# Kernel tuning notes

Hardware: AMD Instinct MI355X
Metric: run time of the kernel (lower is better)

The kernel has to match this reference:

```python
import jax, jax.numpy as jnp
import numpy as np

N = 100000      # nodes (single node type)
R = 4           # relations
E = 800000      # edges per relation (avg in-degree ~32)
D_IN, D_H, D_OUT = 256, 64, 16


def setup_inputs() -> dict:
    key = jax.random.key(0)
    ks = jax.random.split(key, 9)
    x = jax.random.normal(ks[0], (N, D_IN), dtype=jnp.float32)
    src = jax.random.randint(ks[1], (R, E), 0, N, dtype=jnp.int32)
    dst = jax.random.randint(ks[2], (R, E), 0, N, dtype=jnp.int32)
    s_in = 1.0 / np.sqrt(D_IN)
    s_h = 1.0 / np.sqrt(D_H)
    W1 = jax.random.normal(ks[3], (R, D_IN, D_H), dtype=jnp.float32) * s_in
    L1w = jax.random.normal(ks[4], (D_IN, D_H), dtype=jnp.float32) * s_in
    L1b = jnp.zeros((D_H,), dtype=jnp.float32)
    W2 = jax.random.normal(ks[5], (R, D_H, D_OUT), dtype=jnp.float32) * s_h
    L2w = jax.random.normal(ks[6], (D_H, D_OUT), dtype=jnp.float32) * s_h
    L2b = jnp.zeros((D_OUT,), dtype=jnp.float32)
    return {"x": x, "src": src, "dst": dst, "W1": W1, "L1w": L1w,
            "L1b": L1b, "W2": W2, "L2w": L2w, "L2b": L2b}


def _rel_graph_conv(h, src, dst, W):
    """Per-relation GEMM + gather + scatter-add + right-normalize, summed over relations.
    h: [N, d_in]; src/dst: [R, E]; W: [R, d_in, d_out] -> [N, d_out]
    """
    hw = jnp.einsum('nd,rdh->rnh', h, W)  # transform first (d_out small), then gather

    def agg(hr, s, d):
        deg = jax.ops.segment_sum(jnp.ones((E,), hr.dtype), d, num_segments=N)
        msg = jax.ops.segment_sum(hr[s], d, num_segments=N)  # [N, d_out]
        return msg / jnp.maximum(deg, 1.0)[:, None]          # norm='right'

    return jnp.sum(jax.vmap(agg)(hw, src, dst), axis=0)


def reference(x, src, dst, W1, L1w, L1b, W2, L2w, L2b):
    # Layer 1: relation conv + self-loop linear + ReLU (dropout = eval/identity)
    h = _rel_graph_conv(x, src, dst, W1) + x @ L1w + L1b
    h = jax.nn.relu(h)
    # Layer 2: no activation
    out = _rel_graph_conv(h, src, dst, W2) + h @ L2w + L2b
    return out
```

## Files before the change

kernel.cpp:

```cpp
#include <hip/hip_runtime.h>


constexpr int NN = 100000, RR = 4, EE = 800000;
constexpr int RE = RR * EE;
constexpr int NBKT = (NN + 63) / 64;
constexpr int BCAP = 3072;
constexpr int NG1 = (NN + 63) / 64;
constexpr int CHUNK = 8192;
constexpr int NB = (RE + CHUNK - 1) / CHUNK;
constexpr int EPT = CHUNK / 512;

typedef short bf16x8 __attribute__((ext_vector_type(8)));
typedef float f32x4 __attribute__((ext_vector_type(4)));

__device__ inline unsigned short f2bf(float f) {
  unsigned u = __float_as_uint(f);
  u += 0x7FFF + ((u >> 16) & 1);
  return (unsigned short)(u >> 16);
}
__device__ inline float bf2f(unsigned short s) {
  return __uint_as_float(((unsigned)s) << 16);
}

__global__ __launch_bounds__(256) void prep_w_kernel(const float* __restrict__ W1,
                                                     const float* __restrict__ L1w,
                                                     const float* __restrict__ W2,
                                                     const float* __restrict__ L2w,
                                                     unsigned short* __restrict__ BT1,
                                                     unsigned short* __restrict__ BT2) {
  int idx = blockIdx.x * 256 + threadIdx.x;
  if (idx < 320 * 256) {
    int n = idx >> 8, k = idx & 255;
    float v = (n < 256) ? W1[((size_t)((n >> 6) * 256 + k)) * 64 + (n & 63)]
                        : L1w[(size_t)k * 64 + (n - 256)];
    BT1[idx] = f2bf(v);
  } else {
    int j = idx - 320 * 256;
    if (j < 80 * 64) {
      int n = j >> 6, k = j & 63;
      float v = (n < 64) ? W2[((size_t)((n >> 4) * 64 + k)) * 16 + (n & 15)]
                         : L2w[(size_t)k * 16 + (n - 64)];
      BT2[j] = f2bf(v);
    }
  }
}

__global__ __launch_bounds__(512) void fused1_kernel(const float* __restrict__ x,
                                                     const unsigned short* __restrict__ BT1,
                                                     const float* __restrict__ L1b,
                                                     const int* __restrict__ src,
                                                     const int* __restrict__ dst,
                                                     int* __restrict__ gcur,
                                                     int* __restrict__ binned,
                                                     unsigned short* __restrict__ hwcat,
                                                     unsigned short* __restrict__ h) {
  __shared__ char lds[49152];
  const int bid = blockIdx.x;
  const int t = threadIdx.x;
  const bool is_bin = (bid % 5 == 0) && (bid / 5 < NB);

  if (is_bin) {
    int* hist = (int*)lds;
    int* base = hist + NBKT;
    for (int k = t; k < NBKT; k += 512) hist[k] = 0;
    __syncthreads();
    const int e0 = (bid / 5) * CHUNK + t;
    int dl[EPT], sl[EPT];
#pragma unroll
    for (int i = 0; i < EPT; ++i) {
      int fl = e0 + i * 512;
      dl[i] = -1;
      if (fl < RE) {
        dl[i] = dst[fl];
        sl[i] = src[fl];
        atomicAdd(&hist[dl[i] >> 6], 1);
      }
    }
    __syncthreads();
    for (int k = t; k < NBKT; k += 512) {
      int hv = hist[k];
      base[k] = hv ? atomicAdd(&gcur[k], hv) : 0;
      hist[k] = 0;
    }
    __syncthreads();
#pragma unroll
    for (int i = 0; i < EPT; ++i) {
      if (dl[i] < 0) continue;
      int fl = e0 + i * 512;
      int r = fl / EE;
      int b = dl[i] >> 6;
      int off = atomicAdd(&hist[b], 1);
      int p = base[b] + off;
      if (p < BCAP) binned[(size_t)b * BCAP + p] = (sl[i] << 2) | r | ((dl[i] & 63) << 19);
    }
    return;
  }

  int nbins = (bid + 4) / 5;
  if (nbins > NB) nbins = NB;
  const int m0 = (bid - nbins) * 64;
  char* Al = lds;
  char* Bl = lds + 64 * 64 * 2;
  const int wid = t >> 6, lane = t & 63;
  const int wm = wid >> 2, wn = wid & 3;
  const int l15 = lane & 15, g = lane >> 4;

  f32x4 acc[2][5];
#pragma unroll
  for (int i = 0; i < 2; ++i)
#pragma unroll
    for (int j = 0; j < 5; ++j) acc[i][j] = (f32x4){0.f, 0.f, 0.f, 0.f};

  for (int kc = 0; kc < 4; ++kc) {
    if (kc) __syncthreads();
#pragma unroll
    for (int it = 0; it < 2; ++it) {
      int fl = t + 512 * it;
      int row = fl >> 4, kq = (fl & 15) * 4;
      int rg = m0 + row;
      float4 v = (rg < NN) ? *(const float4*)(x + (size_t)rg * 256 + kc * 64 + kq)
                           : make_float4(0.f, 0.f, 0.f, 0.f);
      ushort4 pck = {f2bf(v.x), f2bf(v.y), f2bf(v.z), f2bf(v.w)};
      int wb = ((row * 64 + kq) * 2) ^ ((row & 7) << 4);
      *(ushort4*)(Al + wb) = pck;
    }
#pragma unroll
    for (int it = 0; it < 5; ++it) {
      int fl = t + 512 * it;
      int n = fl >> 3, i8 = (fl & 7) * 8;
      uint4 u = *(const uint4*)(BT1 + (size_t)n * 256 + kc * 64 + i8);
      int wb = ((n * 64 + i8) * 2) ^ ((n & 7) << 4);
      *(uint4*)(Bl + wb) = u;
    }
    __syncthreads();
#pragma unroll
    for (int ks = 0; ks < 2; ++ks) {
      bf16x8 af[2], bfr[5];
#pragma unroll
      for (int mi = 0; mi < 2; ++mi) {
        int row = wm * 32 + mi * 16 + l15;
        int byte = ((row * 64 + ks * 32 + g * 8) * 2) ^ ((row & 7) << 4);
        af[mi] = *(const bf16x8*)(Al + byte);
      }
#pragma unroll
      for (int ni = 0; ni < 5; ++ni) {
        int n = wn * 80 + ni * 16 + l15;
        int byte = ((n * 64 + ks * 32 + g * 8) * 2) ^ ((n & 7) << 4);
        bfr[ni] = *(const bf16x8*)(Bl + byte);
      }
#pragma unroll
      for (int mi = 0; mi < 2; ++mi)
#pragma unroll
        for (int ni = 0; ni < 5; ++ni)
          acc[mi][ni] = __builtin_amdgcn_mfma_f32_16x16x32_bf16(af[mi], bfr[ni], acc[mi][ni], 0, 0, 0);
    }
  }
#pragma unroll
  for (int mi = 0; mi < 2; ++mi) {
    int rbase = m0 + wm * 32 + mi * 16 + 4 * g;
#pragma unroll
    for (int ni = 0; ni < 5; ++ni) {
      int n0 = wn * 80 + ni * 16;
      int n = n0 + l15;
#pragma unroll
      for (int e = 0; e < 4; ++e) {
        int row = rbase + e;
        if (row >= NN) continue;
        float v = acc[mi][ni][e];
        if (n0 < 256) hwcat[(size_t)row * 256 + n] = f2bf(v);
        else h[(size_t)row * 64 + (n - 256)] = f2bf(v + L1b[n - 256]);
      }
    }
  }
}

__global__ __launch_bounds__(256) void pull1_kernel(const unsigned short* __restrict__ h,
                                                    const unsigned short* __restrict__ hwcat,
                                                    const int* __restrict__ binned,
                                                    const int* __restrict__ gcur,
                                                    const unsigned short* __restrict__ BT2,
                                                    const float* __restrict__ L2b,
                                                    unsigned short* __restrict__ hw2,
                                                    float* __restrict__ out) {
  __shared__ int csr[BCAP];
  __shared__ int cnt[256];
  __shared__ int off[256];
  __shared__ float winv[256];
  __shared__ int tot[64];
  __shared__ char Al[64 * 64 * 2];
  const int t = threadIdx.x, bkt = blockIdx.x;
  const int wid = t >> 6, lane = t & 63;
  const int l15 = lane & 15, g = lane >> 4;

  int count = gcur[bkt];
  if (count > BCAP) count = BCAP;
  const int* edges = binned + (size_t)bkt * BCAP;

  cnt[t] = 0;
  __syncthreads();
  for (int i = t; i < count; i += 256) {
    int w = edges[i];
    atomicAdd(&cnt[((w >> 19) & 63) * 4 + (w & 3)], 1);
  }
  __syncthreads();
  off[t] = cnt[t];
  __syncthreads();
  for (int s = 1; s < 256; s <<= 1) {
    int v = (t >= s) ? off[t - s] : 0;
    __syncthreads();
    off[t] += v;
    __syncthreads();
  }
  int excl = off[t] - cnt[t];
  winv[t] = 1.0f / (float)(cnt[t] > 1 ? cnt[t] : 1);
  __syncthreads();
  off[t] = excl;
  cnt[t] = excl;
  __syncthreads();
  if (t < 64) tot[t] = ((t == 63) ? count : off[(t + 1) * 4]) - off[t * 4];
  __syncthreads();
  for (int i = t; i < count; i += 256) {
    int w = edges[i];
    int k = ((w >> 19) & 63) * 4 + (w & 3);
    int p = atomicAdd(&cnt[k], 1);
    csr[p] = w & 0x7FFFF;
  }
  __syncthreads();

  const int slot = lane >> 3, cpart = lane & 7;
  for (int ii = 0; ii < 16; ++ii) {
    int nloc = wid * 16 + ii;
    int beg = off[nloc * 4];
    int total = tot[nloc];
    float acc[8] = {0.f, 0.f, 0.f, 0.f, 0.f, 0.f, 0.f, 0.f};
    for (int p0 = 0; p0 < total; p0 += 8) {
      int j = p0 + slot;
      bool pr = j < total;
      int key = pr ? csr[beg + j] : 0;
      float wv = pr ? winv[nloc * 4 + (key & 3)] : 0.f;
      uint4 u = *(const uint4*)(hwcat + (size_t)key * 64 + cpart * 8);
#pragma unroll
      for (int q = 0; q < 4; ++q) {
        unsigned uu = (&u.x)[q];
        acc[q * 2]     = fmaf(wv, bf2f((unsigned short)(uu & 0xffffu)), acc[q * 2]);
        acc[q * 2 + 1] = fmaf(wv, bf2f((unsigned short)(uu >> 16)), acc[q * 2 + 1]);
      }
    }
#pragma unroll
    for (int m = 8; m <= 32; m <<= 1)
#pragma unroll
      for (int q = 0; q < 8; ++q) acc[q] += __shfl_xor(acc[q], m);
    if (slot == 0) {
      int gn = bkt * 64 + nloc;
      unsigned pk[4];
      uint4 hu = make_uint4(0, 0, 0, 0);
      if (gn < NN) hu = *(const uint4*)(h + (size_t)gn * 64 + cpart * 8);
#pragma unroll
      for (int q = 0; q < 4; ++q) {
        unsigned a = (&hu.x)[q];
        float v0 = acc[q * 2]     + bf2f((unsigned short)(a & 0xffffu));
        float v1 = acc[q * 2 + 1] + bf2f((unsigned short)(a >> 16));
        pk[q] = (unsigned)f2bf(fmaxf(v0, 0.f)) | ((unsigned)f2bf(fmaxf(v1, 0.f)) << 16);
      }
      int wb = ((nloc * 64 + cpart * 8) * 2) ^ ((nloc & 7) << 4);
      *(uint4*)(Al + wb) = make_uint4(pk[0], pk[1], pk[2], pk[3]);
    }
  }
  __syncthreads();

  char* Bl = (char*)csr;
#pragma unroll
  for (int it = 0; it < 3; ++it) {
    int fl = t + 256 * it;
    if (fl < 640) {
      int n = fl >> 3, i8 = (fl & 7) * 8;
      uint4 u = *(const uint4*)(BT2 + (size_t)n * 64 + i8);
      int wb = ((n * 64 + i8) * 2) ^ ((n & 7) << 4);
      *(uint4*)(Bl + wb) = u;
    }
  }
  __syncthreads();

  f32x4 acc2[5];
#pragma unroll
  for (int j = 0; j < 5; ++j) acc2[j] = (f32x4){0.f, 0.f, 0.f, 0.f};
#pragma unroll
  for (int ks = 0; ks < 2; ++ks) {
    int ra = wid * 16 + l15;
    int byte = ((ra * 64 + ks * 32 + g * 8) * 2) ^ ((ra & 7) << 4);
    bf16x8 af = *(const bf16x8*)(Al + byte);
#pragma unroll
    for (int ni = 0; ni < 5; ++ni) {
      int n = ni * 16 + l15;
      int nb = ((n * 64 + ks * 32 + g * 8) * 2) ^ ((n & 7) << 4);
      bf16x8 bfr = *(const bf16x8*)(Bl + nb);
      acc2[ni] = __builtin_amdgcn_mfma_f32_16x16x32_bf16(af, bfr, acc2[ni], 0, 0, 0);
    }
  }
  int rb = wid * 16 + 4 * g;
#pragma unroll
  for (int ni = 0; ni < 5; ++ni) {
    int n0 = ni * 16;
    int n = n0 + l15;
#pragma unroll
    for (int e = 0; e < 4; ++e) {
      int gno = bkt * 64 + rb + e;
      if (gno >= NN) continue;
      float vv = acc2[ni][e];
      if (n0 < 64) hw2[(size_t)gno * 64 + n] = f2bf(vv);
      else out[(size_t)gno * 16 + (n - 64)] = vv + L2b[n - 64];
    }
  }
}

__global__ __launch_bounds__(256) void pull2_kernel(const unsigned short* __restrict__ hw2,
                                                    const int* __restrict__ binned,
                                                    const int* __restrict__ gcur,
                                                    float* __restrict__ out) {
  __shared__ int csr[BCAP];
  __shared__ int cnt[256];
  __shared__ int off[256];
  __shared__ float winv[256];
  __shared__ int tot[64];
  __shared__ float ot[64][16];
  const int t = threadIdx.x, bkt = blockIdx.x;
  const int wid = t >> 6, lane = t & 63;

  int count = gcur[bkt];
  if (count > BCAP) count = BCAP;
  const int* edges = binned + (size_t)bkt * BCAP;

  cnt[t] = 0;
  __syncthreads();
  for (int i = t; i < count; i += 256) {
    int w = edges[i];
    atomicAdd(&cnt[((w >> 19) & 63) * 4 + (w & 3)], 1);
  }
  __syncthreads();
  off[t] = cnt[t];
  __syncthreads();
  for (int s = 1; s < 256; s <<= 1) {
    int v = (t >= s) ? off[t - s] : 0;
    __syncthreads();
    off[t] += v;
    __syncthreads();
  }
  int excl = off[t] - cnt[t];
  winv[t] = 1.0f / (float)(cnt[t] > 1 ? cnt[t] : 1);
  __syncthreads();
  off[t] = excl;
  cnt[t] = excl;
  __syncthreads();
  if (t < 64) tot[t] = ((t == 63) ? count : off[(t + 1) * 4]) - off[t * 4];
  __syncthreads();
  for (int i = t; i < count; i += 256) {
    int w = edges[i];
    int k = ((w >> 19) & 63) * 4 + (w & 3);
    int p = atomicAdd(&cnt[k], 1);
    csr[p] = w & 0x7FFFF;
  }
  __syncthreads();

  const int slot = lane >> 2, cpart = lane & 3;
  for (int ii = 0; ii < 16; ++ii) {
    int nloc = wid * 16 + ii;
    int beg = off[nloc * 4];
    int total = tot[nloc];
    float acc[4] = {0.f, 0.f, 0.f, 0.f};
    for (int p0 = 0; p0 < total; p0 += 16) {
      int j = p0 + slot;
      bool pr = j < total;
      int key = pr ? csr[beg + j] : 0;
      float wv = pr ? winv[nloc * 4 + (key & 3)] : 0.f;
      uint2 u = *(const uint2*)(hw2 + (size_t)key * 16 + cpart * 4);
      acc[0] = fmaf(wv, bf2f((unsigned short)(u.x & 0xffffu)), acc[0]);
      acc[1] = fmaf(wv, bf2f((unsigned short)(u.x >> 16)), acc[1]);
      acc[2] = fmaf(wv, bf2f((unsigned short)(u.y & 0xffffu)), acc[2]);
      acc[3] = fmaf(wv, bf2f((unsigned short)(u.y >> 16)), acc[3]);
    }
#pragma unroll
    for (int m = 4; m <= 32; m <<= 1)
#pragma unroll
      for (int q = 0; q < 4; ++q) acc[q] += __shfl_xor(acc[q], m);
    if (slot == 0)
      *(float4*)&ot[nloc][cpart * 4] = make_float4(acc[0], acc[1], acc[2], acc[3]);
  }
  __syncthreads();

  int row = t >> 2, q = t & 3;
  int gn = bkt * 64 + row;
  if (gn < NN) {
    float4 o = *(float4*)(out + (size_t)gn * 16 + q * 4);
    float4 a = *(float4*)&ot[row][q * 4];
    o.x += a.x; o.y += a.y; o.z += a.z; o.w += a.w;
    *(float4*)(out + (size_t)gn * 16 + q * 4) = o;
  }
}

extern "C" void kernel_launch(void* const* d_in, const int* in_sizes, int n_in,
                              void* d_out, int out_size, void* d_ws, size_t ws_size,
                              hipStream_t stream) {
  const float* x   = (const float*)d_in[0];
  const int*   src = (const int*)d_in[1];
  const int*   dst = (const int*)d_in[2];
  const float* W1  = (const float*)d_in[3];
  const float* L1w = (const float*)d_in[4];
  const float* L1b = (const float*)d_in[5];
  const float* W2  = (const float*)d_in[6];
  const float* L2w = (const float*)d_in[7];
  const float* L2b = (const float*)d_in[8];
  float* out = (float*)d_out;

  char* p = (char*)d_ws;
  int* binned = (int*)p;                      p += (size_t)NBKT * BCAP * 4;
  int* gcur   = (int*)p;                      p += 8192;
  unsigned short* hwcat = (unsigned short*)p; p += (size_t)NN * 256 * 2;
  unsigned short* h = (unsigned short*)p;     p += (size_t)NN * 64 * 2;
  unsigned short* hw2 = (unsigned short*)p;   p += (size_t)NN * 64 * 2;
  unsigned short* BT1 = (unsigned short*)p;   p += 320 * 256 * 2;
  unsigned short* BT2 = (unsigned short*)p;   p += 80 * 64 * 2;
  if ((size_t)(p - (char*)d_ws) > ws_size) return;

  hipMemsetAsync(gcur, 0, NBKT * 4, stream);
  prep_w_kernel<<<(320 * 256 + 80 * 64 + 255) / 256, 256, 0, stream>>>(W1, L1w, W2, L2w, BT1, BT2);
  fused1_kernel<<<NG1 + NB, 512, 0, stream>>>(x, BT1, L1b, src, dst, gcur, binned, hwcat, h);
  pull1_kernel<<<NBKT, 256, 0, stream>>>(h, hwcat, binned, gcur, BT2, L2b, hw2, out);
  pull2_kernel<<<NBKT, 256, 0, stream>>>(hw2, binned, gcur, out);
}
```

Before: 229.7 us.

## Prefetch GEMM tiles via direct LDS loads and reuse pull1 CSR in pull2

The layer-1 GEMM now takes B weights pre-swizzled by prep_w and copies them straight into LDS with global_load_lds, and it loads the next x chunk into registers while the current chunk is being multiplied. pull1 replaces its Hillis-Steele shared-memory scan with a wave shuffle scan. It also writes the sorted per-bucket CSR, per-node headers and inverse degrees back to global memory, so pull2 loads them instead of rebuilding the histogram and scatter. The aim is to cut global-to-LDS latency, barriers and repeated CSR construction, at the cost of extra global writes and reads plus more registers for the prefetch.

After: 235.5 us. +2.6%, slower.

```diff
diff --git a/kernel.cpp b/kernel.cpp
--- a/kernel.cpp
+++ b/kernel.cpp
@@ -26,14 +26,16 @@
                                                      const float* __restrict__ L1w,
                                                      const float* __restrict__ W2,
                                                      const float* __restrict__ L2w,
-                                                     unsigned short* __restrict__ BT1,
+                                                     unsigned short* __restrict__ BT1sw,
                                                      unsigned short* __restrict__ BT2) {
   int idx = blockIdx.x * 256 + threadIdx.x;
   if (idx < 320 * 256) {
     int n = idx >> 8, k = idx & 255;
     float v = (n < 256) ? W1[((size_t)((n >> 6) * 256 + k)) * 64 + (n & 63)]
                         : L1w[(size_t)k * 64 + (n - 256)];
-    BT1[idx] = f2bf(v);
+    int kc = k >> 6, c = (k & 63) >> 3, e = k & 7;
+    int byteoff = kc * 40960 + ((n * 128 + c * 16) ^ ((n & 7) << 4)) + e * 2;
+    *(unsigned short*)((char*)BT1sw + byteoff) = f2bf(v);
   } else {
     int j = idx - 320 * 256;
     if (j < 80 * 64) {
@@ -46,7 +48,7 @@
 }
 
 __global__ __launch_bounds__(512) void fused1_kernel(const float* __restrict__ x,
-                                                     const unsigned short* __restrict__ BT1,
+                                                     const unsigned short* __restrict__ BT1sw,
                                                      const float* __restrict__ L1b,
                                                      const int* __restrict__ src,
                                                      const int* __restrict__ dst,
@@ -100,7 +102,7 @@
   if (nbins > NB) nbins = NB;
   const int m0 = (bid - nbins) * 64;
   char* Al = lds;
-  char* Bl = lds + 64 * 64 * 2;
+  char* Bl = lds + 8192;
   const int wid = t >> 6, lane = t & 63;
   const int wm = wid >> 2, wn = wid & 3;
   const int l15 = lane & 15, g = lane >> 4;
@@ -111,28 +113,38 @@
 #pragma unroll
     for (int j = 0; j < 5; ++j) acc[i][j] = (f32x4){0.f, 0.f, 0.f, 0.f};
 
+  const int row0 = t >> 4, kq0 = (t & 15) * 4;
+  const int row1 = (t + 512) >> 4, kq1 = ((t + 512) & 15) * 4;
+  const int rg0 = m0 + row0, rg1 = m0 + row1;
+  const float4 z4 = make_float4(0.f, 0.f, 0.f, 0.f);
+
+  float4 a0 = (rg0 < NN) ? *(const float4*)(x + (size_t)rg0 * 256 + kq0) : z4;
+  float4 a1 = (rg1 < NN) ? *(const float4*)(x + (size_t)rg1 * 256 + kq1) : z4;
+
   for (int kc = 0; kc < 4; ++kc) {
     if (kc) __syncthreads();
-#pragma unroll
-    for (int it = 0; it < 2; ++it) {
-      int fl = t + 512 * it;
-      int row = fl >> 4, kq = (fl & 15) * 4;
-      int rg = m0 + row;
-      float4 v = (rg < NN) ? *(const float4*)(x + (size_t)rg * 256 + kc * 64 + kq)
-                           : make_float4(0.f, 0.f, 0.f, 0.f);
-      ushort4 pck = {f2bf(v.x), f2bf(v.y), f2bf(v.z), f2bf(v.w)};
-      int wb = ((row * 64 + kq) * 2) ^ ((row & 7) << 4);
-      *(ushort4*)(Al + wb) = pck;
-    }
-#pragma unroll
-    for (int it = 0; it < 5; ++it) {
-      int fl = t + 512 * it;
-      int n = fl >> 3, i8 = (fl & 7) * 8;
-      uint4 u = *(const uint4*)(BT1 + (size_t)n * 256 + kc * 64 + i8);
-      int wb = ((n * 64 + i8) * 2) ^ ((n & 7) << 4);
-      *(uint4*)(Bl + wb) = u;
+    {
+      const char* gB = (const char*)BT1sw + kc * 40960;
+#pragma unroll
+      for (int it = 0; it < 5; ++it) {
+        int sl5 = (it * 8 + wid) * 1024;
+        __builtin_amdgcn_global_load_lds((const unsigned int*)(gB + sl5 + lane * 16),
+                                         (unsigned int*)(Bl + sl5), 16, 0, 0);
+      }
+    }
+    {
+      ushort4 p0 = {f2bf(a0.x), f2bf(a0.y), f2bf(a0.z), f2bf(a0.w)};
+      int wb0 = ((row0 * 64 + kq0) * 2) ^ ((row0 & 7) << 4);
+      *(ushort4*)(Al + wb0) = p0;
+      ushort4 p1 = {f2bf(a1.x), f2bf(a1.y), f2bf(a1.z), f2bf(a1.w)};
+      int wb1 = ((row1 * 64 + kq1) * 2) ^ ((row1 & 7) << 4);
+      *(ushort4*)(Al + wb1) = p1;
     }
     __syncthreads();
+    if (kc < 3) {
+      a0 = (rg0 < NN) ? *(const float4*)(x + (size_t)rg0 * 256 + (kc + 1) * 64 + kq0) : z4;
+      a1 = (rg1 < NN) ? *(const float4*)(x + (size_t)rg1 * 256 + (kc + 1) * 64 + kq1) : z4;
+    }
 #pragma unroll
     for (int ks = 0; ks < 2; ++ks) {
       bf16x8 af[2], bfr[5];
@@ -176,10 +188,12 @@
 
 __global__ __launch_bounds__(256) void pull1_kernel(const unsigned short* __restrict__ h,
                                                     const unsigned short* __restrict__ hwcat,
-                                                    const int* __restrict__ binned,
+                                                    int* __restrict__ binned,
                                                     const int* __restrict__ gcur,
                                                     const unsigned short* __restrict__ BT2,
                                                     const float* __restrict__ L2b,
+                                                    unsigned* __restrict__ hdrG,
+                                                    float* __restrict__ winvG,
                                                     unsigned short* __restrict__ hw2,
                                                     float* __restrict__ out) {
   __shared__ int csr[BCAP];
@@ -187,6 +201,7 @@
   __shared__ int off[256];
   __shared__ float winv[256];
   __shared__ int tot[64];
+  __shared__ int wsum[4];
   __shared__ char Al[64 * 64 * 2];
   const int t = threadIdx.x, bkt = blockIdx.x;
   const int wid = t >> 6, lane = t & 63;
@@ -203,22 +218,25 @@
     atomicAdd(&cnt[((w >> 19) & 63) * 4 + (w & 3)], 1);
   }
   __syncthreads();
-  off[t] = cnt[t];
-  __syncthreads();
-  for (int s = 1; s < 256; s <<= 1) {
-    int v = (t >= s) ? off[t - s] : 0;
-    __syncthreads();
-    off[t] += v;
-    __syncthreads();
-  }
-  int excl = off[t] - cnt[t];
-  winv[t] = 1.0f / (float)(cnt[t] > 1 ? cnt[t] : 1);
-  __syncthreads();
+  int v = cnt[t];
+  int xs = v;
+#pragma unroll
+  for (int d = 1; d < 64; d <<= 1) {
+    int y = __shfl_up(xs, d);
+    if (lane >= d) xs += y;
+  }
+  if (lane == 63) wsum[wid] = xs;
+  __syncthreads();
+  int add = 0;
+#pragma unroll
+  for (int w2 = 0; w2 < 4; ++w2)
+    if (w2 < wid) add += wsum[w2];
+  int excl = xs + add - v;
+  winv[t] = 1.0f / (float)(v > 1 ? v : 1);
   off[t] = excl;
   cnt[t] = excl;
   __syncthreads();
   if (t < 64) tot[t] = ((t == 63) ? count : off[(t + 1) * 4]) - off[t * 4];
-  __syncthreads();
   for (int i = t; i < count; i += 256) {
     int w = edges[i];
     int k = ((w >> 19) & 63) * 4 + (w & 3);
@@ -226,6 +244,10 @@
     csr[p] = w & 0x7FFFF;
   }
   __syncthreads();
+
+  for (int i = t; i < count; i += 256) binned[(size_t)bkt * BCAP + i] = csr[i];
+  winvG[bkt * 256 + t] = winv[t];
+  if (t < 64) hdrG[bkt * 64 + t] = (unsigned)off[t * 4] | ((unsigned)tot[t] << 16);
 
   const int slot = lane >> 3, cpart = lane & 7;
   for (int ii = 0; ii < 16; ++ii) {
@@ -316,62 +338,38 @@
 __global__ __launch_bounds__(256) void pull2_kernel(const unsigned short* __restrict__ hw2,
                                                     const int* __restrict__ binned,
                                                     const int* __restrict__ gcur,
+                                                    const unsigned* __restrict__ hdrG,
+                                                    const float* __restrict__ winvG,
                                                     float* __restrict__ out) {
   __shared__ int csr[BCAP];
-  __shared__ int cnt[256];
-  __shared__ int off[256];
-  __shared__ float winv[256];
-  __shared__ int tot[64];
+  __shared__ float winvL[256];
+  __shared__ int begL[64], totL[64];
   __shared__ float ot[64][16];
   const int t = threadIdx.x, bkt = blockIdx.x;
   const int wid = t >> 6, lane = t & 63;
 
   int count = gcur[bkt];
   if (count > BCAP) count = BCAP;
-  const int* edges = binned + (size_t)bkt * BCAP;
-
-  cnt[t] = 0;
-  __syncthreads();
-  for (int i = t; i < count; i += 256) {
-    int w = edges[i];
-    atomicAdd(&cnt[((w >> 19) & 63) * 4 + (w & 3)], 1);
-  }
-  __syncthreads();
-  off[t] = cnt[t];
-  __syncthreads();
-  for (int s = 1; s < 256; s <<= 1) {
-    int v = (t >= s) ? off[t - s] : 0;
-    __syncthreads();
-    off[t] += v;
-    __syncthreads();
-  }
-  int excl = off[t] - cnt[t];
-  winv[t] = 1.0f / (float)(cnt[t] > 1 ? cnt[t] : 1);
-  __syncthreads();
-  off[t] = excl;
-  cnt[t] = excl;
-  __syncthreads();
-  if (t < 64) tot[t] = ((t == 63) ? count : off[(t + 1) * 4]) - off[t * 4];
-  __syncthreads();
-  for (int i = t; i < count; i += 256) {
-    int w = edges[i];
-    int k = ((w >> 19) & 63) * 4 + (w & 3);
-    int p = atomicAdd(&cnt[k], 1);
-    csr[p] = w & 0x7FFFF;
+  for (int i = t; i < count; i += 256) csr[i] = binned[(size_t)bkt * BCAP + i];
+  winvL[t] = winvG[bkt * 256 + t];
+  if (t < 64) {
+    unsigned hd = hdrG[bkt * 64 + t];
+    begL[t] = hd & 0xffff;
+    totL[t] = hd >> 16;
   }
   __syncthreads();
 
   const int slot = lane >> 2, cpart = lane & 3;
   for (int ii = 0; ii < 16; ++ii) {
     int nloc = wid * 16 + ii;
-    int beg = off[nloc * 4];
-    int total = tot[nloc];
+    int beg = begL[nloc];
+    int total = totL[nloc];
     float acc[4] = {0.f, 0.f, 0.f, 0.f};
     for (int p0 = 0; p0 < total; p0 += 16) {
       int j = p0 + slot;
       bool pr = j < total;
       int key = pr ? csr[beg + j] : 0;
-      float wv = pr ? winv[nloc * 4 + (key & 3)] : 0.f;
+      float wv = pr ? winvL[nloc * 4 + (key & 3)] : 0.f;
       uint2 u = *(const uint2*)(hw2 + (size_t)key * 16 + cpart * 4);
       acc[0] = fmaf(wv, bf2f((unsigned short)(u.x & 0xffffu)), acc[0]);
       acc[1] = fmaf(wv, bf2f((unsigned short)(u.x >> 16)), acc[1]);
@@ -417,13 +415,15 @@
   unsigned short* hwcat = (unsigned short*)p; p += (size_t)NN * 256 * 2;
   unsigned short* h = (unsigned short*)p;     p += (size_t)NN * 64 * 2;
   unsigned short* hw2 = (unsigned short*)p;   p += (size_t)NN * 64 * 2;
-  unsigned short* BT1 = (unsigned short*)p;   p += 320 * 256 * 2;
+  unsigned short* BT1sw = (unsigned short*)p; p += 4 * 40960;
   unsigned short* BT2 = (unsigned short*)p;   p += 80 * 64 * 2;
+  unsigned* hdrG = (unsigned*)p;              p += (size_t)NBKT * 64 * 4;
+  float* winvG = (float*)p;                   p += (size_t)NBKT * 256 * 4;
   if ((size_t)(p - (char*)d_ws) > ws_size) return;
 
   hipMemsetAsync(gcur, 0, NBKT * 4, stream);
-  prep_w_kernel<<<(320 * 256 + 80 * 64 + 255) / 256, 256, 0, stream>>>(W1, L1w, W2, L2w, BT1, BT2);
-  fused1_kernel<<<NG1 + NB, 512, 0, stream>>>(x, BT1, L1b, src, dst, gcur, binned, hwcat, h);
-  pull1_kernel<<<NBKT, 256, 0, stream>>>(h, hwcat, binned, gcur, BT2, L2b, hw2, out);
-  pull2_kernel<<<NBKT, 256, 0, stream>>>(hw2, binned, gcur, out);
-}
+  prep_w_kernel<<<(320 * 256 + 80 * 64 + 255) / 256, 256, 0, stream>>>(W1, L1w, W2, L2w, BT1sw, BT2);
+  fused1_kernel<<<NG1 + NB, 512, 0, stream>>>(x, BT1sw, L1b, src, dst, gcur, binned, hwcat, h);
+  pull1_kernel<<<NBKT, 256, 0, stream>>>(h, hwcat, binned, gcur, BT2, L2b, hdrG, winvG, hw2, out);
+  pull2_kernel<<<NBKT, 256, 0, stream>>>(hw2, binned, gcur, hdrG, winvG, out);
+}
```
